# Kernel optimization log

Hardware: AMD Instinct MI355X
Metric: run time of the kernel (lower is better)

The kernel has to match this reference:

```python
import jax, jax.numpy as jnp
import numpy as np

N_NODES = 500_000
N_EDGES = 16_000_000


def setup_inputs() -> dict:
    key = jax.random.key(0)
    ks = jax.random.split(key, 16)
    x = jax.random.normal(ks[0], (N_NODES, 4), dtype=jnp.float32)
    edge_index = jax.random.randint(ks[1], (2, N_EDGES), 0, N_NODES, dtype=jnp.int64)

    def lin(k, out_dim, in_dim):
        # kaiming-uniform-ish init like torch Linear
        bound = 1.0 / np.sqrt(in_dim)
        return jax.random.uniform(k, (out_dim, in_dim), jnp.float32, -bound, bound)

    def bias(k, out_dim, in_dim):
        bound = 1.0 / np.sqrt(in_dim)
        return jax.random.uniform(k, (out_dim,), jnp.float32, -bound, bound)

    return {
        "x": x,
        "edge_index": edge_index,
        # SAGEConv1: 4 -> 10  (lin_l acts on aggregated neighbors, has bias; lin_r on self, no bias)
        "w1l": lin(ks[2], 10, 4), "b1": bias(ks[3], 10, 4), "w1r": lin(ks[4], 10, 4),
        # SAGEConv2: 10 -> 20
        "w2l": lin(ks[5], 20, 10), "b2": bias(ks[6], 20, 10), "w2r": lin(ks[7], 20, 10),
        # SAGEConv3: 20 -> 20
        "w3l": lin(ks[8], 20, 20), "b3": bias(ks[9], 20, 20), "w3r": lin(ks[10], 20, 20),
        # classifier: 20 -> 8
        "wc": lin(ks[11], 8, 20), "bc": bias(ks[12], 8, 20),
    }


def _sage_conv(h, src, dst, deg_inv, wl, bl, wr):
    # mean-aggregate neighbor features: messages flow src -> dst
    msg = h[src]                                   # [E, F] gather
    agg = jax.ops.segment_sum(msg, dst, num_segments=N_NODES)  # [N, F]
    agg = agg * deg_inv                            # mean over in-neighbors
    return agg @ wl.T + bl + h @ wr.T              # lin_l(aggr) + lin_r(self)


def reference(x, edge_index, w1l, b1, w1r, w2l, b2, w2r, w3l, b3, w3r, wc, bc):
    src, dst = edge_index[0], edge_index[1]
    deg = jax.ops.segment_sum(jnp.ones((src.shape[0],), x.dtype), dst,
                              num_segments=N_NODES)
    deg_inv = (1.0 / jnp.maximum(deg, 1.0))[:, None]  # [N, 1]

    h = jax.nn.relu(_sage_conv(x, src, dst, deg_inv, w1l, b1, w1r))
    h = jax.nn.relu(_sage_conv(h, src, dst, deg_inv, w2l, b2, w2r))
    h = jax.nn.relu(_sage_conv(h, src, dst, deg_inv, w3l, b3, w3r))
    return h @ wc.T + bc
```

## Files before the change

### kernel.cpp

```cpp
#include <hip/hip_runtime.h>
#include <hip/hip_fp16.h>

#define N_NODES 500000
#define N_EDGES 16000000
#define NB 1954
#define NPB_LOG 9
#define NPB 512
#define NBUCK 977
#define NBUCK_PAD 1024
#define CH 32768
#define NSB 489

__device__ __forceinline__ float2 up2(int p) {
    __half2 h = *reinterpret_cast<__half2*>(&p);
    return __half22float2(h);
}
__device__ __forceinline__ int pk2(float a, float b) {
    __half2 h = __floats2half2_rn(a, b);
    return *reinterpret_cast<int*>(&h);
}


__global__ void bucket_hist(const int* __restrict__ dst, int* __restrict__ ghist) {
    __shared__ int lhist[NBUCK_PAD];
    for (int t = threadIdx.x; t < NBUCK_PAD; t += 256) lhist[t] = 0;
    __syncthreads();
    int stride = gridDim.x * 256;
    for (int i = blockIdx.x * 256 + threadIdx.x; i < N_EDGES; i += stride) {
        atomicAdd(&lhist[dst[i] >> NPB_LOG], 1);
    }
    __syncthreads();
    for (int t = threadIdx.x; t < NBUCK_PAD; t += 256) {
        int c = lhist[t];
        if (c) atomicAdd(&ghist[t], c);
    }
}

__global__ void bucket_scan(int* __restrict__ gcur, int* __restrict__ bbase) {
    __shared__ int s[256];
    int t = threadIdx.x;
    int v[4], sum = 0, loc[4];
#pragma unroll
    for (int j = 0; j < 4; ++j) {
        v[j] = gcur[t * 4 + j];
        loc[j] = sum;
        sum += v[j];
    }
    s[t] = sum;
    __syncthreads();
    for (int o = 1; o < 256; o <<= 1) {
        int x = (t >= o) ? s[t - o] : 0;
        __syncthreads();
        s[t] += x;
        __syncthreads();
    }
    int excl = s[t] - sum;
#pragma unroll
    for (int j = 0; j < 4; ++j) {
        int e = excl + loc[j];
        bbase[t * 4 + j] = e;
        gcur[t * 4 + j] = e;
    }
    if (t == 255) bbase[NBUCK_PAD] = s[255];
}

__global__ void bucket_scatter(const int* __restrict__ src, const int* __restrict__ dst,
                               int* __restrict__ gcur, int* __restrict__ P) {
    __shared__ int lhist[NBUCK_PAD];
    __shared__ int lcur[NBUCK_PAD];
    for (int t = threadIdx.x; t < NBUCK_PAD; t += 256) lhist[t] = 0;
    __syncthreads();
    int e0 = blockIdx.x * CH;
    int e1 = min(e0 + CH, N_EDGES);
    for (int i = e0 + threadIdx.x; i < e1; i += 256) {
        atomicAdd(&lhist[dst[i] >> NPB_LOG], 1);
    }
    __syncthreads();
    for (int t = threadIdx.x; t < NBUCK_PAD; t += 256) {
        int c = lhist[t];
        lcur[t] = c ? atomicAdd(&gcur[t], c) : 0;
    }
    __syncthreads();
    for (int i = e0 + threadIdx.x; i < e1; i += 256) {
        int d = dst[i];
        int s = src[i];
        int b = d >> NPB_LOG;
        int pos = atomicAdd(&lcur[b], 1);
        P[pos] = ((d & (NPB - 1)) << 19) | s;
    }
}

__global__ void fine_sort(const int* __restrict__ P, const int* __restrict__ bbase,
                          int* __restrict__ off, int* __restrict__ S) {
    __shared__ int lhist[NPB];
    __shared__ int lexcl[NPB];
    __shared__ int sscan[256];
    int t = threadIdx.x;
    int b = blockIdx.x;
    int bb = bbase[b];
    int be = bbase[b + 1];
    int node0 = b << NPB_LOG;

    lhist[t] = 0;
    lhist[t + 256] = 0;
    __syncthreads();
    for (int j = bb + t; j < be; j += 256) {
        atomicAdd(&lhist[P[j] >> 19], 1);
    }
    __syncthreads();

    int a0 = lhist[2 * t], a1 = lhist[2 * t + 1];
    int ps = a0 + a1;
    sscan[t] = ps;
    __syncthreads();
    for (int o = 1; o < 256; o <<= 1) {
        int x = (t >= o) ? sscan[t - o] : 0;
        __syncthreads();
        sscan[t] += x;
        __syncthreads();
    }
    int pe = sscan[t] - ps;
    lexcl[2 * t] = pe;
    lexcl[2 * t + 1] = pe + a0;
    __syncthreads();

#pragma unroll
    for (int j = 0; j < 2; ++j) {
        int idx = t + j * 256;
        int ng = node0 + idx;
        if (ng < N_NODES) off[ng] = bb + lexcl[idx];
        lhist[idx] = lexcl[idx];
    }
    if (b == NBUCK - 1 && t == 0) off[N_NODES] = N_EDGES;
    __syncthreads();

    for (int j = bb + t; j < be; j += 256) {
        int p = P[j];
        int n = p >> 19;
        int s = p & 0x7FFFF;
        int pos = atomicAdd(&lhist[n], 1);
        S[bb + pos] = s;
    }
}


__global__ void convert_x(const float* __restrict__ x, int2* __restrict__ xh) {
    int i = blockIdx.x * 256 + threadIdx.x;
    if (i >= N_NODES) return;
    float4 v = ((const float4*)x)[i];
    int2 r;
    r.x = pk2(v.x, v.y);
    r.y = pk2(v.z, v.w);
    xh[i] = r;
}


__global__ __launch_bounds__(256, 4) void fused_l1(
        const int* __restrict__ off, const int* __restrict__ ssrc,
        const int2* __restrict__ xh, const float* __restrict__ x,
        const float* __restrict__ wl, const float* __restrict__ bl,
        const float* __restrict__ wr, int* __restrict__ h1) {
    __shared__ float s_wl[40];
    __shared__ float s_wr[40];
    __shared__ float s_b[10];
    if (threadIdx.x < 40) {
        s_wl[threadIdx.x] = wl[threadIdx.x];
        s_wr[threadIdx.x] = wr[threadIdx.x];
    }
    if (threadIdx.x >= 64 && threadIdx.x < 74) s_b[threadIdx.x - 64] = bl[threadIdx.x - 64];
    __syncthreads();

    int i = blockIdx.x * 256 + threadIdx.x;
    if (i >= N_NODES) return;

    int b = off[i], e = off[i + 1];
    constexpr int UN = 8;

    float acc[4] = {0.f, 0.f, 0.f, 0.f};

    int k = b;
    for (; k + UN - 1 < e; k += UN) {
        int sidx[UN];
#pragma unroll
        for (int u = 0; u < UN; ++u) sidx[u] = ssrc[k + u];
        int2 v[UN];
#pragma unroll
        for (int u = 0; u < UN; ++u) v[u] = xh[sidx[u]];
#pragma unroll
        for (int u = 0; u < UN; ++u) {
            float2 f0 = up2(v[u].x), f1 = up2(v[u].y);
            acc[0] += f0.x; acc[1] += f0.y; acc[2] += f1.x; acc[3] += f1.y;
        }
    }
    for (; k < e; ++k) {
        int2 v = xh[ssrc[k]];
        float2 f0 = up2(v.x), f1 = up2(v.y);
        acc[0] += f0.x; acc[1] += f0.y; acc[2] += f1.x; acc[3] += f1.y;
    }

    float inv = 1.f / fmaxf((float)(e - b), 1.f);
#pragma unroll
    for (int q = 0; q < 4; ++q) acc[q] *= inv;

    float4 xs = ((const float4*)x)[i];
    float xv[4] = {xs.x, xs.y, xs.z, xs.w};

    float r[10];
#pragma unroll
    for (int j = 0; j < 10; ++j) {
        float t = s_b[j];
#pragma unroll
        for (int kk = 0; kk < 4; ++kk) {
            t += s_wl[j * 4 + kk] * acc[kk] + s_wr[j * 4 + kk] * xv[kk];
        }
        r[j] = fmaxf(t, 0.f);
    }
    int4 o0;
    o0.x = pk2(r[0], r[1]); o0.y = pk2(r[2], r[3]);
    o0.z = pk2(r[4], r[5]); o0.w = pk2(r[6], r[7]);
    *(int4*)(h1 + (long)i * 8) = o0;
    h1[(long)i * 8 + 4] = pk2(r[8], r[9]);
}

__global__ __launch_bounds__(256, 4) void fused_l2(
        const int* __restrict__ off, const int* __restrict__ ssrc,
        const int* __restrict__ h1,
        const float* __restrict__ wl, const float* __restrict__ bl,
        const float* __restrict__ wr, int* __restrict__ h2) {
    __shared__ float s_wl[200];
    __shared__ float s_wr[200];
    __shared__ float s_b[20];
    if (threadIdx.x < 200) {
        s_wl[threadIdx.x] = wl[threadIdx.x];
        s_wr[threadIdx.x] = wr[threadIdx.x];
    }
    if (threadIdx.x >= 224 && threadIdx.x < 244) s_b[threadIdx.x - 224] = bl[threadIdx.x - 224];
    __syncthreads();

    int i = blockIdx.x * 256 + threadIdx.x;
    if (i >= N_NODES) return;

    int b = off[i], e = off[i + 1];
    constexpr int UN = 4;

    float acc[10];
#pragma unroll
    for (int q = 0; q < 10; ++q) acc[q] = 0.f;

    int k = b;
    for (; k + UN - 1 < e; k += UN) {
        int sidx[UN];
#pragma unroll
        for (int u = 0; u < UN; ++u) sidx[u] = ssrc[k + u];
        int4 v4[UN];
        int v1[UN];
#pragma unroll
        for (int u = 0; u < UN; ++u) {
            const int* row = h1 + (long)sidx[u] * 8;
            v4[u] = *(const int4*)row;
            v1[u] = row[4];
        }
#pragma unroll
        for (int u = 0; u < UN; ++u) {
            float2 f0 = up2(v4[u].x), f1 = up2(v4[u].y), f2 = up2(v4[u].z), f3 = up2(v4[u].w), f4 = up2(v1[u]);
            acc[0] += f0.x; acc[1] += f0.y; acc[2] += f1.x; acc[3] += f1.y;
            acc[4] += f2.x; acc[5] += f2.y; acc[6] += f3.x; acc[7] += f3.y;
            acc[8] += f4.x; acc[9] += f4.y;
        }
    }
    for (; k < e; ++k) {
        const int* row = h1 + (long)ssrc[k] * 8;
        int4 v4 = *(const int4*)row;
        int v1 = row[4];
        float2 f0 = up2(v4.x), f1 = up2(v4.y), f2 = up2(v4.z), f3 = up2(v4.w), f4 = up2(v1);
        acc[0] += f0.x; acc[1] += f0.y; acc[2] += f1.x; acc[3] += f1.y;
        acc[4] += f2.x; acc[5] += f2.y; acc[6] += f3.x; acc[7] += f3.y;
        acc[8] += f4.x; acc[9] += f4.y;
    }

    float inv = 1.f / fmaxf((float)(e - b), 1.f);
#pragma unroll
    for (int q = 0; q < 10; ++q) acc[q] *= inv;

    float xv[10];
    {
        const int* row = h1 + (long)i * 8;
        int4 v4 = *(const int4*)row;
        int v1 = row[4];
        float2 f0 = up2(v4.x), f1 = up2(v4.y), f2 = up2(v4.z), f3 = up2(v4.w), f4 = up2(v1);
        xv[0] = f0.x; xv[1] = f0.y; xv[2] = f1.x; xv[3] = f1.y;
        xv[4] = f2.x; xv[5] = f2.y; xv[6] = f3.x; xv[7] = f3.y;
        xv[8] = f4.x; xv[9] = f4.y;
    }

    float r[20];
#pragma unroll
    for (int j = 0; j < 20; ++j) {
        float t = s_b[j];
#pragma unroll
        for (int kk = 0; kk < 10; ++kk) {
            t += s_wl[j * 10 + kk] * acc[kk] + s_wr[j * 10 + kk] * xv[kk];
        }
        r[j] = fmaxf(t, 0.f);
    }
    int* o = h2 + (long)i * 16;
    int4 o0, o1;
    o0.x = pk2(r[0], r[1]);   o0.y = pk2(r[2], r[3]);
    o0.z = pk2(r[4], r[5]);   o0.w = pk2(r[6], r[7]);
    o1.x = pk2(r[8], r[9]);   o1.y = pk2(r[10], r[11]);
    o1.z = pk2(r[12], r[13]); o1.w = pk2(r[14], r[15]);
    *(int4*)o = o0;
    *(int4*)(o + 4) = o1;
    int2 o2;
    o2.x = pk2(r[16], r[17]); o2.y = pk2(r[18], r[19]);
    *(int2*)(o + 8) = o2;
}

__global__ __launch_bounds__(256, 4) void fused_l3(
        const int* __restrict__ off, const int* __restrict__ ssrc,
        const int* __restrict__ h2,
        const float* __restrict__ w3l, const float* __restrict__ b3,
        const float* __restrict__ w3r,
        const float* __restrict__ wc, const float* __restrict__ bc,
        float* __restrict__ out) {
    __shared__ float s_wl[400];
    __shared__ float s_wr[400];
    __shared__ float s_b[20];
    __shared__ float s_wc[160];
    __shared__ float s_bc[8];
    for (int t = threadIdx.x; t < 400; t += 256) {
        s_wl[t] = w3l[t];
        s_wr[t] = w3r[t];
    }
    if (threadIdx.x < 160) s_wc[threadIdx.x] = wc[threadIdx.x];
    if (threadIdx.x >= 192 && threadIdx.x < 212) s_b[threadIdx.x - 192] = b3[threadIdx.x - 192];
    if (threadIdx.x >= 224 && threadIdx.x < 232) s_bc[threadIdx.x - 224] = bc[threadIdx.x - 224];
    __syncthreads();

    int i = blockIdx.x * 256 + threadIdx.x;
    if (i >= N_NODES) return;

    int b = off[i], e = off[i + 1];
    constexpr int UN = 4;

    float acc[20];
#pragma unroll
    for (int q = 0; q < 20; ++q) acc[q] = 0.f;

    int k = b;
    for (; k + UN - 1 < e; k += UN) {
        int sidx[UN];
#pragma unroll
        for (int u = 0; u < UN; ++u) sidx[u] = ssrc[k + u];
        int4 va[UN], vb[UN];
        int2 vc[UN];
#pragma unroll
        for (int u = 0; u < UN; ++u) {
            const int* row = h2 + (long)sidx[u] * 16;
            va[u] = *(const int4*)row;
            vb[u] = *(const int4*)(row + 4);
            vc[u] = *(const int2*)(row + 8);
        }
#pragma unroll
        for (int u = 0; u < UN; ++u) {
            float2 f;
            f = up2(va[u].x); acc[0] += f.x; acc[1] += f.y;
            f = up2(va[u].y); acc[2] += f.x; acc[3] += f.y;
            f = up2(va[u].z); acc[4] += f.x; acc[5] += f.y;
            f = up2(va[u].w); acc[6] += f.x; acc[7] += f.y;
            f = up2(vb[u].x); acc[8] += f.x; acc[9] += f.y;
            f = up2(vb[u].y); acc[10] += f.x; acc[11] += f.y;
            f = up2(vb[u].z); acc[12] += f.x; acc[13] += f.y;
            f = up2(vb[u].w); acc[14] += f.x; acc[15] += f.y;
            f = up2(vc[u].x); acc[16] += f.x; acc[17] += f.y;
            f = up2(vc[u].y); acc[18] += f.x; acc[19] += f.y;
        }
    }
    for (; k < e; ++k) {
        const int* row = h2 + (long)ssrc[k] * 16;
        int4 va = *(const int4*)row;
        int4 vb = *(const int4*)(row + 4);
        int2 vc = *(const int2*)(row + 8);
        float2 f;
        f = up2(va.x); acc[0] += f.x; acc[1] += f.y;
        f = up2(va.y); acc[2] += f.x; acc[3] += f.y;
        f = up2(va.z); acc[4] += f.x; acc[5] += f.y;
        f = up2(va.w); acc[6] += f.x; acc[7] += f.y;
        f = up2(vb.x); acc[8] += f.x; acc[9] += f.y;
        f = up2(vb.y); acc[10] += f.x; acc[11] += f.y;
        f = up2(vb.z); acc[12] += f.x; acc[13] += f.y;
        f = up2(vb.w); acc[14] += f.x; acc[15] += f.y;
        f = up2(vc.x); acc[16] += f.x; acc[17] += f.y;
        f = up2(vc.y); acc[18] += f.x; acc[19] += f.y;
    }

    float inv = 1.f / fmaxf((float)(e - b), 1.f);
#pragma unroll
    for (int q = 0; q < 20; ++q) acc[q] *= inv;

    float xv[20];
    {
        const int* row = h2 + (long)i * 16;
        int4 va = *(const int4*)row;
        int4 vb = *(const int4*)(row + 4);
        int2 vc = *(const int2*)(row + 8);
        float2 f;
        f = up2(va.x); xv[0] = f.x; xv[1] = f.y;
        f = up2(va.y); xv[2] = f.x; xv[3] = f.y;
        f = up2(va.z); xv[4] = f.x; xv[5] = f.y;
        f = up2(va.w); xv[6] = f.x; xv[7] = f.y;
        f = up2(vb.x); xv[8] = f.x; xv[9] = f.y;
        f = up2(vb.y); xv[10] = f.x; xv[11] = f.y;
        f = up2(vb.z); xv[12] = f.x; xv[13] = f.y;
        f = up2(vb.w); xv[14] = f.x; xv[15] = f.y;
        f = up2(vc.x); xv[16] = f.x; xv[17] = f.y;
        f = up2(vc.y); xv[18] = f.x; xv[19] = f.y;
    }

    float h3[20];
#pragma unroll
    for (int j = 0; j < 20; ++j) {
        float r = s_b[j];
#pragma unroll
        for (int kk = 0; kk < 20; ++kk) {
            r += s_wl[j * 20 + kk] * acc[kk] + s_wr[j * 20 + kk] * xv[kk];
        }
        h3[j] = fmaxf(r, 0.f);
    }
#pragma unroll
    for (int j = 0; j < 8; ++j) {
        float r = s_bc[j];
#pragma unroll
        for (int kk = 0; kk < 20; ++kk) {
            r += s_wc[j * 20 + kk] * h3[kk];
        }
        out[(long)i * 8 + j] = r;
    }
}


__global__ void deg_kernel(const int* __restrict__ dst, int* __restrict__ deg) {
    int i = blockIdx.x * blockDim.x + threadIdx.x;
    if (i < N_EDGES) atomicAdd(&deg[dst[i]], 1);
}

template <int F>
__global__ void edge_agg(const int* __restrict__ src, const int* __restrict__ dst,
                         const float* __restrict__ h, float* __restrict__ agg) {
    int i = blockIdx.x * blockDim.x + threadIdx.x;
    if (i >= N_EDGES) return;
    int s = src[i];
    int d = dst[i];
    const float* hs = h + (long)s * F;
    float* ad = agg + (long)d * F;
#pragma unroll
    for (int f = 0; f < F; ++f) atomicAdd(&ad[f], hs[f]);
}

template <int FIN, int FOUT>
__global__ void node_apply(const float* __restrict__ agg, const float* __restrict__ hin,
                           const int* __restrict__ deg, const float* __restrict__ wl,
                           const float* __restrict__ bl, const float* __restrict__ wr,
                           float* __restrict__ hout) {
    __shared__ float s_wl[FOUT * FIN];
    __shared__ float s_wr[FOUT * FIN];
    __shared__ float s_b[FOUT];
    for (int t = threadIdx.x; t < FOUT * FIN; t += blockDim.x) {
        s_wl[t] = wl[t];
        s_wr[t] = wr[t];
    }
    for (int t = threadIdx.x; t < FOUT; t += blockDim.x) s_b[t] = bl[t];
    __syncthreads();
    int i = blockIdx.x * blockDim.x + threadIdx.x;
    if (i >= N_NODES) return;
    float inv = 1.0f / fmaxf((float)deg[i], 1.0f);
    float a[FIN], xv[FIN];
#pragma unroll
    for (int kk = 0; kk < FIN; ++kk) {
        a[kk] = agg[(long)i * FIN + kk] * inv;
        xv[kk] = hin[(long)i * FIN + kk];
    }
#pragma unroll
    for (int j = 0; j < FOUT; ++j) {
        float r = s_b[j];
#pragma unroll
        for (int kk = 0; kk < FIN; ++kk) r += s_wl[j * FIN + kk] * a[kk] + s_wr[j * FIN + kk] * xv[kk];
        hout[(long)i * FOUT + j] = fmaxf(r, 0.f);
    }
}

__global__ void node_final_old(const float* __restrict__ agg, const float* __restrict__ hin,
                               const int* __restrict__ deg, const float* __restrict__ w3l,
                               const float* __restrict__ b3, const float* __restrict__ w3r,
                               const float* __restrict__ wc, const float* __restrict__ bc,
                               float* __restrict__ out) {
    __shared__ float s_wl[400];
    __shared__ float s_wr[400];
    __shared__ float s_b[20];
    __shared__ float s_wc[160];
    __shared__ float s_bc[8];
    for (int t = threadIdx.x; t < 400; t += blockDim.x) {
        s_wl[t] = w3l[t];
        s_wr[t] = w3r[t];
    }
    for (int t = threadIdx.x; t < 160; t += blockDim.x) s_wc[t] = wc[t];
    for (int t = threadIdx.x; t < 20; t += blockDim.x) s_b[t] = b3[t];
    for (int t = threadIdx.x; t < 8; t += blockDim.x) s_bc[t] = bc[t];
    __syncthreads();
    int i = blockIdx.x * blockDim.x + threadIdx.x;
    if (i >= N_NODES) return;
    float inv = 1.0f / fmaxf((float)deg[i], 1.0f);
    float a[20], xv[20];
#pragma unroll
    for (int kk = 0; kk < 20; ++kk) {
        a[kk] = agg[(long)i * 20 + kk] * inv;
        xv[kk] = hin[(long)i * 20 + kk];
    }
    float h3[20];
#pragma unroll
    for (int j = 0; j < 20; ++j) {
        float r = s_b[j];
#pragma unroll
        for (int kk = 0; kk < 20; ++kk) r += s_wl[j * 20 + kk] * a[kk] + s_wr[j * 20 + kk] * xv[kk];
        h3[j] = fmaxf(r, 0.f);
    }
#pragma unroll
    for (int j = 0; j < 8; ++j) {
        float r = s_bc[j];
#pragma unroll
        for (int kk = 0; kk < 20; ++kk) r += s_wc[j * 20 + kk] * h3[kk];
        out[(long)i * 8 + j] = r;
    }
}


extern "C" void kernel_launch(void* const* d_in, const int* in_sizes, int n_in,
                              void* d_out, int out_size, void* d_ws, size_t ws_size,
                              hipStream_t stream) {
    const float* x = (const float*)d_in[0];
    const int* ei = (const int*)d_in[1];
    const float* w1l = (const float*)d_in[2];
    const float* b1 = (const float*)d_in[3];
    const float* w1r = (const float*)d_in[4];
    const float* w2l = (const float*)d_in[5];
    const float* b2 = (const float*)d_in[6];
    const float* w2r = (const float*)d_in[7];
    const float* w3l = (const float*)d_in[8];
    const float* b3 = (const float*)d_in[9];
    const float* w3r = (const float*)d_in[10];
    const float* wc = (const float*)d_in[11];
    const float* bc = (const float*)d_in[12];
    float* out = (float*)d_out;

    const int* src = ei;
    const int* dst = ei + N_EDGES;

    const int BT = 256;
    dim3 blk(BT);
    dim3 egrid((N_EDGES + BT - 1) / BT);
    dim3 ngrid(NB);

    const size_t NEED_A = 130008448;

    if (ws_size >= NEED_A) {
        char* ws = (char*)d_ws;
        int* off = (int*)ws;
        int* bbase = (int*)(ws + 2000128);
        int* gcur = (int*)(ws + 2004352);
        int* P = (int*)(ws + 2008448);
        int2* xh = (int2*)(ws + 2008448);
        int* h1 = (int*)(ws + 6008448);
        int* h2 = (int*)(ws + 22008448);
        int* S = (int*)(ws + 66008448);

        hipMemsetAsync(gcur, 0, NBUCK_PAD * sizeof(int), stream);
        bucket_hist<<<1024, blk, 0, stream>>>(dst, gcur);
        bucket_scan<<<1, blk, 0, stream>>>(gcur, bbase);
        bucket_scatter<<<NSB, blk, 0, stream>>>(src, dst, gcur, P);
        fine_sort<<<NBUCK, blk, 0, stream>>>(P, bbase, off, S);

        convert_x<<<ngrid, blk, 0, stream>>>(x, xh);
        fused_l1<<<ngrid, blk, 0, stream>>>(off, S, xh, x, w1l, b1, w1r, h1);
        fused_l2<<<ngrid, blk, 0, stream>>>(off, S, h1, w2l, b2, w2r, h2);
        fused_l3<<<ngrid, blk, 0, stream>>>(off, S, h2, w3l, b3, w3r, wc, bc, out);
    } else {
        char* ws = (char*)d_ws;
        int* deg = (int*)ws;
        float* agg = (float*)(ws + 2000000);
        float* h1 = (float*)(ws + 42000000);
        float* h2 = (float*)(ws + 62000000);

        hipMemsetAsync(deg, 0, (size_t)N_NODES * sizeof(int), stream);
        deg_kernel<<<egrid, blk, 0, stream>>>(dst, deg);

        hipMemsetAsync(agg, 0, (size_t)N_NODES * 4 * sizeof(float), stream);
        edge_agg<4><<<egrid, blk, 0, stream>>>(src, dst, x, agg);
        node_apply<4, 10><<<ngrid, blk, 0, stream>>>(agg, x, deg, w1l, b1, w1r, h1);

        hipMemsetAsync(agg, 0, (size_t)N_NODES * 10 * sizeof(float), stream);
        edge_agg<10><<<egrid, blk, 0, stream>>>(src, dst, h1, agg);
        node_apply<10, 20><<<ngrid, blk, 0, stream>>>(agg, h1, deg, w2l, b2, w2r, h2);

        hipMemsetAsync(agg, 0, (size_t)N_NODES * 20 * sizeof(float), stream);
        edge_agg<20><<<egrid, blk, 0, stream>>>(src, dst, h2, agg);
        node_final_old<<<ngrid, blk, 0, stream>>>(agg, h2, deg, w3l, b3, w3r, wc, bc, out);
    }
}
```

Measured before the change: 1.661 ms.

## Replace per-node CSR sort with source-tiled buckets and LDS atomic aggregation

Drops the fine per-node counting sort and CSR offsets. Each 512-node destination bucket is instead reordered by coarse source tile, and each layer aggregates its bucket with shared-memory float atomics, one block per bucket, computing degree in LDS. The goal is a cheaper sort and gathers with better source locality. The cost is many LDS atomics per edge (up to 21), non-deterministic float summation order, and only 977 blocks with large LDS footprints, which lowers occupancy.

```diff
diff --git a/kernel.cpp b/kernel.cpp
--- a/kernel.cpp
+++ b/kernel.cpp
@@ -10,6 +10,7 @@
 #define NBUCK_PAD 1024
 #define CH 32768
 #define NSB 489
+#define TILE_LOG 15
 
 __device__ __forceinline__ float2 up2(int p) {
     __half2 h = *reinterpret_cast<__half2*>(&p);
@@ -90,56 +91,31 @@
     }
 }
 
-__global__ void fine_sort(const int* __restrict__ P, const int* __restrict__ bbase,
-                          int* __restrict__ off, int* __restrict__ S) {
-    __shared__ int lhist[NPB];
-    __shared__ int lexcl[NPB];
-    __shared__ int sscan[256];
-    int t = threadIdx.x;
-    int b = blockIdx.x;
-    int bb = bbase[b];
-    int be = bbase[b + 1];
-    int node0 = b << NPB_LOG;
-
-    lhist[t] = 0;
-    lhist[t + 256] = 0;
+__global__ void tile_sort(const int* __restrict__ P, const int* __restrict__ bbase,
+                          int* __restrict__ P2) {
+    __shared__ int h16[16];
+    __shared__ int c16[16];
+    int t = threadIdx.x, b = blockIdx.x;
+    int bb = bbase[b], be = bbase[b + 1];
+    if (t < 16) h16[t] = 0;
     __syncthreads();
     for (int j = bb + t; j < be; j += 256) {
-        atomicAdd(&lhist[P[j] >> 19], 1);
-    }
-    __syncthreads();
-
-    int a0 = lhist[2 * t], a1 = lhist[2 * t + 1];
-    int ps = a0 + a1;
-    sscan[t] = ps;
-    __syncthreads();
-    for (int o = 1; o < 256; o <<= 1) {
-        int x = (t >= o) ? sscan[t - o] : 0;
-        __syncthreads();
-        sscan[t] += x;
-        __syncthreads();
-    }
-    int pe = sscan[t] - ps;
-    lexcl[2 * t] = pe;
-    lexcl[2 * t + 1] = pe + a0;
-    __syncthreads();
-
-#pragma unroll
-    for (int j = 0; j < 2; ++j) {
-        int idx = t + j * 256;
-        int ng = node0 + idx;
-        if (ng < N_NODES) off[ng] = bb + lexcl[idx];
-        lhist[idx] = lexcl[idx];
-    }
-    if (b == NBUCK - 1 && t == 0) off[N_NODES] = N_EDGES;
-    __syncthreads();
-
+        atomicAdd(&h16[(P[j] & 0x7FFFF) >> TILE_LOG], 1);
+    }
+    __syncthreads();
+    if (t == 0) {
+        int s = 0;
+#pragma unroll
+        for (int i = 0; i < 16; ++i) {
+            c16[i] = s;
+            s += h16[i];
+        }
+    }
+    __syncthreads();
     for (int j = bb + t; j < be; j += 256) {
         int p = P[j];
-        int n = p >> 19;
-        int s = p & 0x7FFFF;
-        int pos = atomicAdd(&lhist[n], 1);
-        S[bb + pos] = s;
+        int pos = atomicAdd(&c16[(p & 0x7FFFF) >> TILE_LOG], 1);
+        P2[bb + pos] = p;
     }
 }
 
@@ -155,286 +131,322 @@
 }
 
 
-__global__ __launch_bounds__(256, 4) void fused_l1(
-        const int* __restrict__ off, const int* __restrict__ ssrc,
-        const int2* __restrict__ xh, const float* __restrict__ x,
-        const float* __restrict__ wl, const float* __restrict__ bl,
-        const float* __restrict__ wr, int* __restrict__ h1) {
-    __shared__ float s_wl[40];
-    __shared__ float s_wr[40];
-    __shared__ float s_b[10];
-    if (threadIdx.x < 40) {
-        s_wl[threadIdx.x] = wl[threadIdx.x];
-        s_wr[threadIdx.x] = wr[threadIdx.x];
-    }
-    if (threadIdx.x >= 64 && threadIdx.x < 74) s_b[threadIdx.x - 64] = bl[threadIdx.x - 64];
-    __syncthreads();
-
-    int i = blockIdx.x * 256 + threadIdx.x;
-    if (i >= N_NODES) return;
-
-    int b = off[i], e = off[i + 1];
-    constexpr int UN = 8;
-
-    float acc[4] = {0.f, 0.f, 0.f, 0.f};
-
-    int k = b;
-    for (; k + UN - 1 < e; k += UN) {
-        int sidx[UN];
-#pragma unroll
-        for (int u = 0; u < UN; ++u) sidx[u] = ssrc[k + u];
-        int2 v[UN];
-#pragma unroll
-        for (int u = 0; u < UN; ++u) v[u] = xh[sidx[u]];
-#pragma unroll
-        for (int u = 0; u < UN; ++u) {
+__global__ void agg_l1(const int* __restrict__ P2, const int* __restrict__ bbase,
+                       const int2* __restrict__ xh, const float* __restrict__ x,
+                       const float* __restrict__ wl, const float* __restrict__ bl,
+                       const float* __restrict__ wr, int* __restrict__ h1) {
+    __shared__ float lacc[NPB * 5];
+    __shared__ int ldeg[NPB];
+    __shared__ float s_wl[40], s_wr[40], s_b[10];
+    int t = threadIdx.x, b = blockIdx.x;
+    for (int k = t; k < NPB * 5; k += 256) lacc[k] = 0.f;
+    ldeg[t] = 0;
+    ldeg[t + 256] = 0;
+    if (t < 40) {
+        s_wl[t] = wl[t];
+        s_wr[t] = wr[t];
+    }
+    if (t >= 64 && t < 74) s_b[t - 64] = bl[t - 64];
+    __syncthreads();
+
+    int bb = bbase[b], be = bbase[b + 1];
+    int j = bb + t;
+    for (; j + 768 < be; j += 1024) {
+        int p[4];
+        p[0] = P2[j]; p[1] = P2[j + 256]; p[2] = P2[j + 512]; p[3] = P2[j + 768];
+        int2 v[4];
+#pragma unroll
+        for (int u = 0; u < 4; ++u) v[u] = xh[p[u] & 0x7FFFF];
+#pragma unroll
+        for (int u = 0; u < 4; ++u) {
+            int dl = p[u] >> 19;
             float2 f0 = up2(v[u].x), f1 = up2(v[u].y);
-            acc[0] += f0.x; acc[1] += f0.y; acc[2] += f1.x; acc[3] += f1.y;
-        }
-    }
-    for (; k < e; ++k) {
-        int2 v = xh[ssrc[k]];
+            float* a = &lacc[dl * 5];
+            atomicAdd(a + 0, f0.x); atomicAdd(a + 1, f0.y);
+            atomicAdd(a + 2, f1.x); atomicAdd(a + 3, f1.y);
+            atomicAdd(&ldeg[dl], 1);
+        }
+    }
+    for (; j < be; j += 256) {
+        int p = P2[j];
+        int dl = p >> 19;
+        int2 v = xh[p & 0x7FFFF];
         float2 f0 = up2(v.x), f1 = up2(v.y);
-        acc[0] += f0.x; acc[1] += f0.y; acc[2] += f1.x; acc[3] += f1.y;
-    }
-
-    float inv = 1.f / fmaxf((float)(e - b), 1.f);
-#pragma unroll
-    for (int q = 0; q < 4; ++q) acc[q] *= inv;
-
-    float4 xs = ((const float4*)x)[i];
-    float xv[4] = {xs.x, xs.y, xs.z, xs.w};
-
-    float r[10];
-#pragma unroll
-    for (int j = 0; j < 10; ++j) {
-        float t = s_b[j];
-#pragma unroll
-        for (int kk = 0; kk < 4; ++kk) {
-            t += s_wl[j * 4 + kk] * acc[kk] + s_wr[j * 4 + kk] * xv[kk];
-        }
-        r[j] = fmaxf(t, 0.f);
-    }
-    int4 o0;
-    o0.x = pk2(r[0], r[1]); o0.y = pk2(r[2], r[3]);
-    o0.z = pk2(r[4], r[5]); o0.w = pk2(r[6], r[7]);
-    *(int4*)(h1 + (long)i * 8) = o0;
-    h1[(long)i * 8 + 4] = pk2(r[8], r[9]);
-}
-
-__global__ __launch_bounds__(256, 4) void fused_l2(
-        const int* __restrict__ off, const int* __restrict__ ssrc,
-        const int* __restrict__ h1,
-        const float* __restrict__ wl, const float* __restrict__ bl,
-        const float* __restrict__ wr, int* __restrict__ h2) {
-    __shared__ float s_wl[200];
-    __shared__ float s_wr[200];
-    __shared__ float s_b[20];
-    if (threadIdx.x < 200) {
-        s_wl[threadIdx.x] = wl[threadIdx.x];
-        s_wr[threadIdx.x] = wr[threadIdx.x];
-    }
-    if (threadIdx.x >= 224 && threadIdx.x < 244) s_b[threadIdx.x - 224] = bl[threadIdx.x - 224];
-    __syncthreads();
-
-    int i = blockIdx.x * 256 + threadIdx.x;
-    if (i >= N_NODES) return;
-
-    int b = off[i], e = off[i + 1];
-    constexpr int UN = 4;
-
-    float acc[10];
-#pragma unroll
-    for (int q = 0; q < 10; ++q) acc[q] = 0.f;
-
-    int k = b;
-    for (; k + UN - 1 < e; k += UN) {
-        int sidx[UN];
-#pragma unroll
-        for (int u = 0; u < UN; ++u) sidx[u] = ssrc[k + u];
-        int4 v4[UN];
-        int v1[UN];
-#pragma unroll
-        for (int u = 0; u < UN; ++u) {
-            const int* row = h1 + (long)sidx[u] * 8;
-            v4[u] = *(const int4*)row;
-            v1[u] = row[4];
-        }
-#pragma unroll
-        for (int u = 0; u < UN; ++u) {
-            float2 f0 = up2(v4[u].x), f1 = up2(v4[u].y), f2 = up2(v4[u].z), f3 = up2(v4[u].w), f4 = up2(v1[u]);
-            acc[0] += f0.x; acc[1] += f0.y; acc[2] += f1.x; acc[3] += f1.y;
-            acc[4] += f2.x; acc[5] += f2.y; acc[6] += f3.x; acc[7] += f3.y;
-            acc[8] += f4.x; acc[9] += f4.y;
-        }
-    }
-    for (; k < e; ++k) {
-        const int* row = h1 + (long)ssrc[k] * 8;
-        int4 v4 = *(const int4*)row;
-        int v1 = row[4];
-        float2 f0 = up2(v4.x), f1 = up2(v4.y), f2 = up2(v4.z), f3 = up2(v4.w), f4 = up2(v1);
-        acc[0] += f0.x; acc[1] += f0.y; acc[2] += f1.x; acc[3] += f1.y;
-        acc[4] += f2.x; acc[5] += f2.y; acc[6] += f3.x; acc[7] += f3.y;
-        acc[8] += f4.x; acc[9] += f4.y;
-    }
-
-    float inv = 1.f / fmaxf((float)(e - b), 1.f);
-#pragma unroll
-    for (int q = 0; q < 10; ++q) acc[q] *= inv;
-
-    float xv[10];
-    {
-        const int* row = h1 + (long)i * 8;
-        int4 v4 = *(const int4*)row;
-        int v1 = row[4];
-        float2 f0 = up2(v4.x), f1 = up2(v4.y), f2 = up2(v4.z), f3 = up2(v4.w), f4 = up2(v1);
-        xv[0] = f0.x; xv[1] = f0.y; xv[2] = f1.x; xv[3] = f1.y;
-        xv[4] = f2.x; xv[5] = f2.y; xv[6] = f3.x; xv[7] = f3.y;
-        xv[8] = f4.x; xv[9] = f4.y;
-    }
-
-    float r[20];
-#pragma unroll
-    for (int j = 0; j < 20; ++j) {
-        float t = s_b[j];
-#pragma unroll
-        for (int kk = 0; kk < 10; ++kk) {
-            t += s_wl[j * 10 + kk] * acc[kk] + s_wr[j * 10 + kk] * xv[kk];
-        }
-        r[j] = fmaxf(t, 0.f);
-    }
-    int* o = h2 + (long)i * 16;
-    int4 o0, o1;
-    o0.x = pk2(r[0], r[1]);   o0.y = pk2(r[2], r[3]);
-    o0.z = pk2(r[4], r[5]);   o0.w = pk2(r[6], r[7]);
-    o1.x = pk2(r[8], r[9]);   o1.y = pk2(r[10], r[11]);
-    o1.z = pk2(r[12], r[13]); o1.w = pk2(r[14], r[15]);
-    *(int4*)o = o0;
-    *(int4*)(o + 4) = o1;
-    int2 o2;
-    o2.x = pk2(r[16], r[17]); o2.y = pk2(r[18], r[19]);
-    *(int2*)(o + 8) = o2;
-}
-
-__global__ __launch_bounds__(256, 4) void fused_l3(
-        const int* __restrict__ off, const int* __restrict__ ssrc,
-        const int* __restrict__ h2,
-        const float* __restrict__ w3l, const float* __restrict__ b3,
-        const float* __restrict__ w3r,
-        const float* __restrict__ wc, const float* __restrict__ bc,
-        float* __restrict__ out) {
-    __shared__ float s_wl[400];
-    __shared__ float s_wr[400];
-    __shared__ float s_b[20];
-    __shared__ float s_wc[160];
-    __shared__ float s_bc[8];
-    for (int t = threadIdx.x; t < 400; t += 256) {
-        s_wl[t] = w3l[t];
-        s_wr[t] = w3r[t];
-    }
-    if (threadIdx.x < 160) s_wc[threadIdx.x] = wc[threadIdx.x];
-    if (threadIdx.x >= 192 && threadIdx.x < 212) s_b[threadIdx.x - 192] = b3[threadIdx.x - 192];
-    if (threadIdx.x >= 224 && threadIdx.x < 232) s_bc[threadIdx.x - 224] = bc[threadIdx.x - 224];
-    __syncthreads();
-
-    int i = blockIdx.x * 256 + threadIdx.x;
-    if (i >= N_NODES) return;
-
-    int b = off[i], e = off[i + 1];
-    constexpr int UN = 4;
-
-    float acc[20];
-#pragma unroll
-    for (int q = 0; q < 20; ++q) acc[q] = 0.f;
-
-    int k = b;
-    for (; k + UN - 1 < e; k += UN) {
-        int sidx[UN];
-#pragma unroll
-        for (int u = 0; u < UN; ++u) sidx[u] = ssrc[k + u];
-        int4 va[UN], vb[UN];
-        int2 vc[UN];
-#pragma unroll
-        for (int u = 0; u < UN; ++u) {
-            const int* row = h2 + (long)sidx[u] * 16;
+        float* a = &lacc[dl * 5];
+        atomicAdd(a + 0, f0.x); atomicAdd(a + 1, f0.y);
+        atomicAdd(a + 2, f1.x); atomicAdd(a + 3, f1.y);
+        atomicAdd(&ldeg[dl], 1);
+    }
+    __syncthreads();
+
+    int node0 = b << NPB_LOG;
+#pragma unroll
+    for (int h = 0; h < 2; ++h) {
+        int dl = t + h * 256;
+        int node = node0 + dl;
+        if (node >= N_NODES) continue;
+        float inv = 1.f / fmaxf((float)ldeg[dl], 1.f);
+        float a[4];
+#pragma unroll
+        for (int q = 0; q < 4; ++q) a[q] = lacc[dl * 5 + q] * inv;
+        float4 xs = ((const float4*)x)[node];
+        float xv[4] = {xs.x, xs.y, xs.z, xs.w};
+        float r[10];
+#pragma unroll
+        for (int jj = 0; jj < 10; ++jj) {
+            float s = s_b[jj];
+#pragma unroll
+            for (int kk = 0; kk < 4; ++kk) {
+                s += s_wl[jj * 4 + kk] * a[kk] + s_wr[jj * 4 + kk] * xv[kk];
+            }
+            r[jj] = fmaxf(s, 0.f);
+        }
+        int4 o0;
+        o0.x = pk2(r[0], r[1]); o0.y = pk2(r[2], r[3]);
+        o0.z = pk2(r[4], r[5]); o0.w = pk2(r[6], r[7]);
+        *(int4*)(h1 + (long)node * 8) = o0;
+        h1[(long)node * 8 + 4] = pk2(r[8], r[9]);
+    }
+}
+
+__global__ void agg_l2(const int* __restrict__ P2, const int* __restrict__ bbase,
+                       const int* __restrict__ h1,
+                       const float* __restrict__ wl, const float* __restrict__ bl,
+                       const float* __restrict__ wr, int* __restrict__ h2) {
+    __shared__ float lacc[NPB * 11];
+    __shared__ int ldeg[NPB];
+    __shared__ float s_wl[200], s_wr[200], s_b[20];
+    int t = threadIdx.x, b = blockIdx.x;
+    for (int k = t; k < NPB * 11; k += 256) lacc[k] = 0.f;
+    ldeg[t] = 0;
+    ldeg[t + 256] = 0;
+    if (t < 200) {
+        s_wl[t] = wl[t];
+        s_wr[t] = wr[t];
+    }
+    if (t >= 224 && t < 244) s_b[t - 224] = bl[t - 224];
+    __syncthreads();
+
+    int bb = bbase[b], be = bbase[b + 1];
+    int j = bb + t;
+    for (; j + 768 < be; j += 1024) {
+        int p[4];
+        p[0] = P2[j]; p[1] = P2[j + 256]; p[2] = P2[j + 512]; p[3] = P2[j + 768];
+        int4 va[4];
+        int vb[4];
+#pragma unroll
+        for (int u = 0; u < 4; ++u) {
+            const int* row = h1 + (long)(p[u] & 0x7FFFF) * 8;
             va[u] = *(const int4*)row;
-            vb[u] = *(const int4*)(row + 4);
-            vc[u] = *(const int2*)(row + 8);
-        }
-#pragma unroll
-        for (int u = 0; u < UN; ++u) {
+            vb[u] = row[4];
+        }
+#pragma unroll
+        for (int u = 0; u < 4; ++u) {
+            int dl = p[u] >> 19;
+            float* a = &lacc[dl * 11];
+            float2 f0 = up2(va[u].x), f1 = up2(va[u].y), f2 = up2(va[u].z), f3 = up2(va[u].w), f4 = up2(vb[u]);
+            atomicAdd(a + 0, f0.x); atomicAdd(a + 1, f0.y);
+            atomicAdd(a + 2, f1.x); atomicAdd(a + 3, f1.y);
+            atomicAdd(a + 4, f2.x); atomicAdd(a + 5, f2.y);
+            atomicAdd(a + 6, f3.x); atomicAdd(a + 7, f3.y);
+            atomicAdd(a + 8, f4.x); atomicAdd(a + 9, f4.y);
+            atomicAdd(&ldeg[dl], 1);
+        }
+    }
+    for (; j < be; j += 256) {
+        int p = P2[j];
+        int dl = p >> 19;
+        const int* row = h1 + (long)(p & 0x7FFFF) * 8;
+        int4 va = *(const int4*)row;
+        int vb = row[4];
+        float* a = &lacc[dl * 11];
+        float2 f0 = up2(va.x), f1 = up2(va.y), f2 = up2(va.z), f3 = up2(va.w), f4 = up2(vb);
+        atomicAdd(a + 0, f0.x); atomicAdd(a + 1, f0.y);
+        atomicAdd(a + 2, f1.x); atomicAdd(a + 3, f1.y);
+        atomicAdd(a + 4, f2.x); atomicAdd(a + 5, f2.y);
+        atomicAdd(a + 6, f3.x); atomicAdd(a + 7, f3.y);
+        atomicAdd(a + 8, f4.x); atomicAdd(a + 9, f4.y);
+        atomicAdd(&ldeg[dl], 1);
+    }
+    __syncthreads();
+
+    int node0 = b << NPB_LOG;
+#pragma unroll
+    for (int h = 0; h < 2; ++h) {
+        int dl = t + h * 256;
+        int node = node0 + dl;
+        if (node >= N_NODES) continue;
+        float inv = 1.f / fmaxf((float)ldeg[dl], 1.f);
+        float a[10];
+#pragma unroll
+        for (int q = 0; q < 10; ++q) a[q] = lacc[dl * 11 + q] * inv;
+        float xv[10];
+        {
+            const int* row = h1 + (long)node * 8;
+            int4 va = *(const int4*)row;
+            int vb = row[4];
+            float2 f0 = up2(va.x), f1 = up2(va.y), f2 = up2(va.z), f3 = up2(va.w), f4 = up2(vb);
+            xv[0] = f0.x; xv[1] = f0.y; xv[2] = f1.x; xv[3] = f1.y;
+            xv[4] = f2.x; xv[5] = f2.y; xv[6] = f3.x; xv[7] = f3.y;
+            xv[8] = f4.x; xv[9] = f4.y;
+        }
+        float r[20];
+#pragma unroll
+        for (int jj = 0; jj < 20; ++jj) {
+            float s = s_b[jj];
+#pragma unroll
+            for (int kk = 0; kk < 10; ++kk) {
+                s += s_wl[jj * 10 + kk] * a[kk] + s_wr[jj * 10 + kk] * xv[kk];
+            }
+            r[jj] = fmaxf(s, 0.f);
+        }
+        int* o = h2 + (long)node * 16;
+        int4 o0, o1;
+        o0.x = pk2(r[0], r[1]);   o0.y = pk2(r[2], r[3]);
+        o0.z = pk2(r[4], r[5]);   o0.w = pk2(r[6], r[7]);
+        o1.x = pk2(r[8], r[9]);   o1.y = pk2(r[10], r[11]);
+        o1.z = pk2(r[12], r[13]); o1.w = pk2(r[14], r[15]);
+        *(int4*)o = o0;
+        *(int4*)(o + 4) = o1;
+        int2 o2;
+        o2.x = pk2(r[16], r[17]); o2.y = pk2(r[18], r[19]);
+        *(int2*)(o + 8) = o2;
+    }
+}
+
+__global__ void agg_l3(const int* __restrict__ P2, const int* __restrict__ bbase,
+                       const int* __restrict__ h2,
+                       const float* __restrict__ w3l, const float* __restrict__ b3,
+                       const float* __restrict__ w3r,
+                       const float* __restrict__ wc, const float* __restrict__ bc,
+                       float* __restrict__ out) {
+    __shared__ float lacc[NPB * 21];
+    __shared__ int ldeg[NPB];
+    __shared__ float s_wl[400], s_wr[400], s_b[20], s_wc[160], s_bc[8];
+    int t = threadIdx.x, b = blockIdx.x;
+    for (int k = t; k < NPB * 21; k += 256) lacc[k] = 0.f;
+    ldeg[t] = 0;
+    ldeg[t + 256] = 0;
+    for (int k = t; k < 400; k += 256) {
+        s_wl[k] = w3l[k];
+        s_wr[k] = w3r[k];
+    }
+    if (t < 160) s_wc[t] = wc[t];
+    if (t >= 192 && t < 212) s_b[t - 192] = b3[t - 192];
+    if (t >= 224 && t < 232) s_bc[t - 224] = bc[t - 224];
+    __syncthreads();
+
+    int bb = bbase[b], be = bbase[b + 1];
+    int j = bb + t;
+    for (; j + 256 < be; j += 512) {
+        int p0 = P2[j], p1 = P2[j + 256];
+        const int* r0 = h2 + (long)(p0 & 0x7FFFF) * 16;
+        const int* r1 = h2 + (long)(p1 & 0x7FFFF) * 16;
+        int4 va0 = *(const int4*)r0, vb0 = *(const int4*)(r0 + 4);
+        int2 vc0 = *(const int2*)(r0 + 8);
+        int4 va1 = *(const int4*)r1, vb1 = *(const int4*)(r1 + 4);
+        int2 vc1 = *(const int2*)(r1 + 8);
+        {
+            int dl = p0 >> 19;
+            float* a = &lacc[dl * 21];
             float2 f;
-            f = up2(va[u].x); acc[0] += f.x; acc[1] += f.y;
-            f = up2(va[u].y); acc[2] += f.x; acc[3] += f.y;
-            f = up2(va[u].z); acc[4] += f.x; acc[5] += f.y;
-            f = up2(va[u].w); acc[6] += f.x; acc[7] += f.y;
-            f = up2(vb[u].x); acc[8] += f.x; acc[9] += f.y;
-            f = up2(vb[u].y); acc[10] += f.x; acc[11] += f.y;
-            f = up2(vb[u].z); acc[12] += f.x; acc[13] += f.y;
-            f = up2(vb[u].w); acc[14] += f.x; acc[15] += f.y;
-            f = up2(vc[u].x); acc[16] += f.x; acc[17] += f.y;
-            f = up2(vc[u].y); acc[18] += f.x; acc[19] += f.y;
-        }
-    }
-    for (; k < e; ++k) {
-        const int* row = h2 + (long)ssrc[k] * 16;
-        int4 va = *(const int4*)row;
-        int4 vb = *(const int4*)(row + 4);
+            f = up2(va0.x); atomicAdd(a + 0, f.x);  atomicAdd(a + 1, f.y);
+            f = up2(va0.y); atomicAdd(a + 2, f.x);  atomicAdd(a + 3, f.y);
+            f = up2(va0.z); atomicAdd(a + 4, f.x);  atomicAdd(a + 5, f.y);
+            f = up2(va0.w); atomicAdd(a + 6, f.x);  atomicAdd(a + 7, f.y);
+            f = up2(vb0.x); atomicAdd(a + 8, f.x);  atomicAdd(a + 9, f.y);
+            f = up2(vb0.y); atomicAdd(a + 10, f.x); atomicAdd(a + 11, f.y);
+            f = up2(vb0.z); atomicAdd(a + 12, f.x); atomicAdd(a + 13, f.y);
+            f = up2(vb0.w); atomicAdd(a + 14, f.x); atomicAdd(a + 15, f.y);
+            f = up2(vc0.x); atomicAdd(a + 16, f.x); atomicAdd(a + 17, f.y);
+            f = up2(vc0.y); atomicAdd(a + 18, f.x); atomicAdd(a + 19, f.y);
+            atomicAdd(&ldeg[dl], 1);
+        }
+        {
+            int dl = p1 >> 19;
+            float* a = &lacc[dl * 21];
+            float2 f;
+            f = up2(va1.x); atomicAdd(a + 0, f.x);  atomicAdd(a + 1, f.y);
+            f = up2(va1.y); atomicAdd(a + 2, f.x);  atomicAdd(a + 3, f.y);
+            f = up2(va1.z); atomicAdd(a + 4, f.x);  atomicAdd(a + 5, f.y);
+            f = up2(va1.w); atomicAdd(a + 6, f.x);  atomicAdd(a + 7, f.y);
+            f = up2(vb1.x); atomicAdd(a + 8, f.x);  atomicAdd(a + 9, f.y);
+            f = up2(vb1.y); atomicAdd(a + 10, f.x); atomicAdd(a + 11, f.y);
+            f = up2(vb1.z); atomicAdd(a + 12, f.x); atomicAdd(a + 13, f.y);
+            f = up2(vb1.w); atomicAdd(a + 14, f.x); atomicAdd(a + 15, f.y);
+            f = up2(vc1.x); atomicAdd(a + 16, f.x); atomicAdd(a + 17, f.y);
+            f = up2(vc1.y); atomicAdd(a + 18, f.x); atomicAdd(a + 19, f.y);
+            atomicAdd(&ldeg[dl], 1);
+        }
+    }
+    for (; j < be; j += 256) {
+        int p = P2[j];
+        int dl = p >> 19;
+        const int* row = h2 + (long)(p & 0x7FFFF) * 16;
+        int4 va = *(const int4*)row, vb = *(const int4*)(row + 4);
         int2 vc = *(const int2*)(row + 8);
+        float* a = &lacc[dl * 21];
         float2 f;
-        f = up2(va.x); acc[0] += f.x; acc[1] += f.y;
-        f = up2(va.y); acc[2] += f.x; acc[3] += f.y;
-        f = up2(va.z); acc[4] += f.x; acc[5] += f.y;
-        f = up2(va.w); acc[6] += f.x; acc[7] += f.y;
-        f = up2(vb.x); acc[8] += f.x; acc[9] += f.y;
-        f = up2(vb.y); acc[10] += f.x; acc[11] += f.y;
-        f = up2(vb.z); acc[12] += f.x; acc[13] += f.y;
-        f = up2(vb.w); acc[14] += f.x; acc[15] += f.y;
-        f = up2(vc.x); acc[16] += f.x; acc[17] += f.y;
-        f = up2(vc.y); acc[18] += f.x; acc[19] += f.y;
-    }
-
-    float inv = 1.f / fmaxf((float)(e - b), 1.f);
-#pragma unroll
-    for (int q = 0; q < 20; ++q) acc[q] *= inv;
-
-    float xv[20];
-    {
-        const int* row = h2 + (long)i * 16;
-        int4 va = *(const int4*)row;
-        int4 vb = *(const int4*)(row + 4);
-        int2 vc = *(const int2*)(row + 8);
-        float2 f;
-        f = up2(va.x); xv[0] = f.x; xv[1] = f.y;
-        f = up2(va.y); xv[2] = f.x; xv[3] = f.y;
-        f = up2(va.z); xv[4] = f.x; xv[5] = f.y;
-        f = up2(va.w); xv[6] = f.x; xv[7] = f.y;
-        f = up2(vb.x); xv[8] = f.x; xv[9] = f.y;
-        f = up2(vb.y); xv[10] = f.x; xv[11] = f.y;
-        f = up2(vb.z); xv[12] = f.x; xv[13] = f.y;
-        f = up2(vb.w); xv[14] = f.x; xv[15] = f.y;
-        f = up2(vc.x); xv[16] = f.x; xv[17] = f.y;
-        f = up2(vc.y); xv[18] = f.x; xv[19] = f.y;
-    }
-
-    float h3[20];
-#pragma unroll
-    for (int j = 0; j < 20; ++j) {
-        float r = s_b[j];
-#pragma unroll
-        for (int kk = 0; kk < 20; ++kk) {
-            r += s_wl[j * 20 + kk] * acc[kk] + s_wr[j * 20 + kk] * xv[kk];
-        }
-        h3[j] = fmaxf(r, 0.f);
-    }
-#pragma unroll
-    for (int j = 0; j < 8; ++j) {
-        float r = s_bc[j];
-#pragma unroll
-        for (int kk = 0; kk < 20; ++kk) {
-            r += s_wc[j * 20 + kk] * h3[kk];
-        }
-        out[(long)i * 8 + j] = r;
+        f = up2(va.x); atomicAdd(a + 0, f.x);  atomicAdd(a + 1, f.y);
+        f = up2(va.y); atomicAdd(a + 2, f.x);  atomicAdd(a + 3, f.y);
+        f = up2(va.z); atomicAdd(a + 4, f.x);  atomicAdd(a + 5, f.y);
+        f = up2(va.w); atomicAdd(a + 6, f.x);  atomicAdd(a + 7, f.y);
+        f = up2(vb.x); atomicAdd(a + 8, f.x);  atomicAdd(a + 9, f.y);
+        f = up2(vb.y); atomicAdd(a + 10, f.x); atomicAdd(a + 11, f.y);
+        f = up2(vb.z); atomicAdd(a + 12, f.x); atomicAdd(a + 13, f.y);
+        f = up2(vb.w); atomicAdd(a + 14, f.x); atomicAdd(a + 15, f.y);
+        f = up2(vc.x); atomicAdd(a + 16, f.x); atomicAdd(a + 17, f.y);
+        f = up2(vc.y); atomicAdd(a + 18, f.x); atomicAdd(a + 19, f.y);
+        atomicAdd(&ldeg[dl], 1);
+    }
+    __syncthreads();
+
+    int node0 = b << NPB_LOG;
+#pragma unroll
+    for (int h = 0; h < 2; ++h) {
+        int dl = t + h * 256;
+        int node = node0 + dl;
+        if (node >= N_NODES) continue;
+        float inv = 1.f / fmaxf((float)ldeg[dl], 1.f);
+        float a[20];
+#pragma unroll
+        for (int q = 0; q < 20; ++q) a[q] = lacc[dl * 21 + q] * inv;
+        float xv[20];
+        {
+            const int* row = h2 + (long)node * 16;
+            int4 va = *(const int4*)row, vb = *(const int4*)(row + 4);
+            int2 vc = *(const int2*)(row + 8);
+            float2 f;
+            f = up2(va.x); xv[0] = f.x;  xv[1] = f.y;
+            f = up2(va.y); xv[2] = f.x;  xv[3] = f.y;
+            f = up2(va.z); xv[4] = f.x;  xv[5] = f.y;
+            f = up2(va.w); xv[6] = f.x;  xv[7] = f.y;
+            f = up2(vb.x); xv[8] = f.x;  xv[9] = f.y;
+            f = up2(vb.y); xv[10] = f.x; xv[11] = f.y;
+            f = up2(vb.z); xv[12] = f.x; xv[13] = f.y;
+            f = up2(vb.w); xv[14] = f.x; xv[15] = f.y;
+            f = up2(vc.x); xv[16] = f.x; xv[17] = f.y;
+            f = up2(vc.y); xv[18] = f.x; xv[19] = f.y;
+        }
+        float h3[20];
+#pragma unroll
+        for (int jj = 0; jj < 20; ++jj) {
+            float r = s_b[jj];
+#pragma unroll
+            for (int kk = 0; kk < 20; ++kk) {
+                r += s_wl[jj * 20 + kk] * a[kk] + s_wr[jj * 20 + kk] * xv[kk];
+            }
+            h3[jj] = fmaxf(r, 0.f);
+        }
+#pragma unroll
+        for (int jj = 0; jj < 8; ++jj) {
+            float r = s_bc[jj];
+#pragma unroll
+            for (int kk = 0; kk < 20; ++kk) {
+                r += s_wc[jj * 20 + kk] * h3[kk];
+            }
+            out[(long)node * 8 + jj] = r;
+        }
     }
 }
 
@@ -559,30 +571,30 @@
     dim3 blk(BT);
     dim3 egrid((N_EDGES + BT - 1) / BT);
     dim3 ngrid(NB);
-
-    const size_t NEED_A = 130008448;
+    dim3 bgrid(NBUCK);
+
+    const size_t NEED_A = 128008448;
 
     if (ws_size >= NEED_A) {
         char* ws = (char*)d_ws;
-        int* off = (int*)ws;
-        int* bbase = (int*)(ws + 2000128);
-        int* gcur = (int*)(ws + 2004352);
-        int* P = (int*)(ws + 2008448);
-        int2* xh = (int2*)(ws + 2008448);
-        int* h1 = (int*)(ws + 6008448);
-        int* h2 = (int*)(ws + 22008448);
-        int* S = (int*)(ws + 66008448);
+        int* bbase = (int*)ws;
+        int* gcur = (int*)(ws + 4224);
+        int* P = (int*)(ws + 8448);
+        int2* xh = (int2*)(ws + 8448);
+        int* h1 = (int*)(ws + 4008448);
+        int* h2 = (int*)(ws + 20008448);
+        int* P2 = (int*)(ws + 64008448);
 
         hipMemsetAsync(gcur, 0, NBUCK_PAD * sizeof(int), stream);
         bucket_hist<<<1024, blk, 0, stream>>>(dst, gcur);
         bucket_scan<<<1, blk, 0, stream>>>(gcur, bbase);
         bucket_scatter<<<NSB, blk, 0, stream>>>(src, dst, gcur, P);
-        fine_sort<<<NBUCK, blk, 0, stream>>>(P, bbase, off, S);
+        tile_sort<<<bgrid, blk, 0, stream>>>(P, bbase, P2);
 
         convert_x<<<ngrid, blk, 0, stream>>>(x, xh);
-        fused_l1<<<ngrid, blk, 0, stream>>>(off, S, xh, x, w1l, b1, w1r, h1);
-        fused_l2<<<ngrid, blk, 0, stream>>>(off, S, h1, w2l, b2, w2r, h2);
-        fused_l3<<<ngrid, blk, 0, stream>>>(off, S, h2, w3l, b3, w3r, wc, bc, out);
+        agg_l1<<<bgrid, blk, 0, stream>>>(P2, bbase, xh, x, w1l, b1, w1r, h1);
+        agg_l2<<<bgrid, blk, 0, stream>>>(P2, bbase, h1, w2l, b2, w2r, h2);
+        agg_l3<<<bgrid, blk, 0, stream>>>(P2, bbase, h2, w3l, b3, w3r, wc, bc, out);
     } else {
         char* ws = (char*)d_ws;
         int* deg = (int*)ws;
```

Measured after the change: 3.516 ms. 2.12x slower.
